# Kernel optimization log

Measured on AMD Instinct MI355X. Metric: run time of the kernel, lower is better.

## Reference

```python
import jax, jax.numpy as jnp
import numpy as np

B, S, D, H = 4, 4096, 512, 8


def setup_inputs() -> dict:
    key = jax.random.key(0)
    ks = jax.random.split(key, 9)
    s = 1.0 / np.sqrt(D)
    return {
        "x": jax.random.normal(ks[0], (B, S, D), jnp.float32),
        "Wq": jax.random.normal(ks[1], (D, D), jnp.float32) * s,
        "bq": jax.random.normal(ks[2], (D,), jnp.float32) * 0.02,
        "Wk": jax.random.normal(ks[3], (D, D), jnp.float32) * s,
        "bk": jax.random.normal(ks[4], (D,), jnp.float32) * 0.02,
        "Wv": jax.random.normal(ks[5], (D, D), jnp.float32) * s,
        "bv": jax.random.normal(ks[6], (D,), jnp.float32) * 0.02,
        "Wo": jax.random.normal(ks[7], (H * D, D), jnp.float32) * (1.0 / np.sqrt(H * D)),
        "bo": jax.random.normal(ks[8], (D,), jnp.float32) * 0.02,
        "num_heads": H,
    }


def reference(x, Wq, bq, Wk, bk, Wv, bv, Wo, bo, num_heads):
    # Q/K/V projections (self-attention path; encoder_output=None)
    q = x @ Wq + bq  # [B,S,D]
    k = x @ Wk + bk
    v = x @ Wv + bv
    scale = 1.0 / jnp.sqrt(jnp.asarray(x.shape[-1], x.dtype))
    scores = jnp.einsum("bqd,bkd->bqk", q, k) * scale  # [B,S,S]
    probs = jax.nn.softmax(scores, axis=-1)
    attn = jnp.einsum("bqk,bkd->bqd", probs, v)  # [B,S,D]
    # Original stacks identical heads then torch.cat along dim=-1 -> tile H copies.
    cat = jnp.tile(attn, (1, 1, num_heads))  # [B,S,H*D]
    return cat @ Wo + bo  # [B,S,D]
```

## Files before the change

kernel.cpp:

```cpp
#include <hip/hip_runtime.h>
#include <stdint.h>

#define SCALE 0.04419417382415922f

typedef __bf16 bf16x8 __attribute__((ext_vector_type(8)));
typedef float f32x4 __attribute__((ext_vector_type(4)));
typedef uint16_t u16x8 __attribute__((ext_vector_type(8)));

static __device__ __forceinline__ uint16_t f2bf(float f) {
  union { float f; uint32_t u; } v; v.f = f;
  uint32_t u = v.u;
  return (uint16_t)((u + 0x7FFFu + ((u >> 16) & 1u)) >> 16);
}
static __device__ __forceinline__ float bf2f(uint16_t h) {
  union { uint32_t u; float f; } v; v.u = ((uint32_t)h) << 16;
  return v.f;
}

static __device__ __forceinline__ void gload16(const void* g, void* l) {
  __builtin_amdgcn_global_load_lds(
      (__attribute__((address_space(1))) void*)g,
      (__attribute__((address_space(3))) void*)l, 16, 0, 0);
}

#define P_BAR asm volatile("s_barrier" ::: "memory")
#define P_LGKM do { asm volatile("s_waitcnt lgkmcnt(0)" ::: "memory"); \
                    __builtin_amdgcn_sched_barrier(0); } while (0)


__global__ __launch_bounds__(256)
void convert_x(const float* __restrict__ x, uint16_t* __restrict__ xb) {
  size_t i = ((size_t)blockIdx.x * 256 + threadIdx.x) * 8;
  float4 a = *(const float4*)(x + i);
  float4 b = *(const float4*)(x + i + 4);
  u16x8 o;
  o[0] = f2bf(a.x); o[1] = f2bf(a.y); o[2] = f2bf(a.z); o[3] = f2bf(a.w);
  o[4] = f2bf(b.x); o[5] = f2bf(b.y); o[6] = f2bf(b.z); o[7] = f2bf(b.w);
  *(u16x8*)(xb + i) = o;
}

__global__ __launch_bounds__(256)
void pack_wraw(const float* __restrict__ Wq, const float* __restrict__ Wk,
               const float* __restrict__ Wv,
               uint16_t* __restrict__ oq, uint16_t* __restrict__ ok,
               uint16_t* __restrict__ ov) {
  size_t i = ((size_t)blockIdx.x * 256 + threadIdx.x) * 8;
  const int m = blockIdx.y;
  const float* src = (m == 0) ? Wq : ((m == 1) ? Wk : Wv);
  uint16_t* dst = (m == 0) ? oq : ((m == 1) ? ok : ov);
  const float scl = (m == 0) ? SCALE : 1.0f;
  float4 a = *(const float4*)(src + i);
  float4 b = *(const float4*)(src + i + 4);
  u16x8 o;
  o[0] = f2bf(a.x * scl); o[1] = f2bf(a.y * scl);
  o[2] = f2bf(a.z * scl); o[3] = f2bf(a.w * scl);
  o[4] = f2bf(b.x * scl); o[5] = f2bf(b.y * scl);
  o[6] = f2bf(b.z * scl); o[7] = f2bf(b.w * scl);
  *(u16x8*)(dst + i) = o;
}

__global__ __launch_bounds__(256)
void pack_wo(const float* __restrict__ Wo, uint16_t* __restrict__ woT) {
  __shared__ float tile[64][65];
  const int k0 = blockIdx.x * 64, n0 = blockIdx.y * 64;
  const int t = threadIdx.x, r = t >> 2, c0 = (t & 3) * 16;
  float av[16];
  #pragma unroll
  for (int e = 0; e < 16; e++) av[e] = 0.f;
  for (int h = 0; h < 8; h++) {
    const float* src = &Wo[(size_t)(h * 512 + k0 + r) * 512 + n0 + c0];
    #pragma unroll
    for (int j = 0; j < 4; j++) {
      float4 v = *(const float4*)(src + j * 4);
      av[j * 4 + 0] += v.x; av[j * 4 + 1] += v.y;
      av[j * 4 + 2] += v.z; av[j * 4 + 3] += v.w;
    }
  }
  #pragma unroll
  for (int e = 0; e < 16; e++) tile[r][c0 + e] = av[e];
  __syncthreads();
  u16x8 o0, o1;
  #pragma unroll
  for (int e = 0; e < 8; e++) {
    o0[e] = f2bf(tile[c0 + e][r]);
    o1[e] = f2bf(tile[c0 + 8 + e][r]);
  }
  uint16_t* dst = woT + (size_t)(n0 + r) * 512 + k0 + c0;
  *(u16x8*)dst = o0;
  *(u16x8*)(dst + 8) = o1;
}

__global__ __launch_bounds__(256)
void gemv_g(const float* __restrict__ Wk, const float* __restrict__ bq,
            float* __restrict__ g) {
  __shared__ float vs[512];
  const int t = threadIdx.x;
  vs[t] = bq[t]; vs[t + 256] = bq[t + 256];
  __syncthreads();
  const int r = blockIdx.x * 32 + (t >> 3), j = t & 7;
  const float4* p = (const float4*)(Wk + (size_t)r * 512 + j * 64);
  float s = 0.f;
  #pragma unroll
  for (int q = 0; q < 16; q++) {
    float4 v = p[q];
    const float* b = &vs[j * 64 + q * 4];
    s += v.x * b[0] + v.y * b[1] + v.z * b[2] + v.w * b[3];
  }
  s += __shfl_xor(s, 1); s += __shfl_xor(s, 2); s += __shfl_xor(s, 4);
  if (j == 0) g[r] = s * SCALE;
}

__global__ __launch_bounds__(256)
void kappa_calc(const float* __restrict__ bq, const float* __restrict__ bk,
                float* __restrict__ g) {
  const int t = threadIdx.x;
  float s = bq[t] * bk[t] + bq[t + 256] * bk[t + 256];
  #pragma unroll
  for (int o = 32; o; o >>= 1) s += __shfl_xor(s, o);
  __shared__ float rr[4];
  if ((t & 63) == 0) rr[t >> 6] = s;
  __syncthreads();
  if (t == 0) g[512] = (rr[0] + rr[1] + rr[2] + rr[3]) * SCALE;
}

__global__ __launch_bounds__(256)
void gemv_bvo(const uint16_t* __restrict__ woT, const float* __restrict__ bv,
              float* __restrict__ out) {
  __shared__ float vs[512];
  const int t = threadIdx.x;
  vs[t] = bv[t]; vs[t + 256] = bv[t + 256];
  __syncthreads();
  const int r = blockIdx.x * 32 + (t >> 3), j = t & 7;
  const u16x8* p = (const u16x8*)(woT + (size_t)r * 512 + j * 64);
  float s = 0.f;
  #pragma unroll
  for (int q = 0; q < 8; q++) {
    u16x8 v = p[q];
    #pragma unroll
    for (int e = 0; e < 8; e++) s += bf2f(v[e]) * vs[j * 64 + q * 8 + e];
  }
  s += __shfl_xor(s, 1); s += __shfl_xor(s, 2); s += __shfl_xor(s, 4);
  if (j == 0) out[r] = s;
}

__global__ __launch_bounds__(256)
void c_vec(const uint16_t* __restrict__ xb, const float* __restrict__ g,
           float* __restrict__ cv) {
  __shared__ float gs[513];
  const int t = threadIdx.x;
  for (int i = t; i < 513; i += 256) gs[i] = g[i];
  __syncthreads();
  const int r = blockIdx.x * 32 + (t >> 3);
  const int j = t & 7;
  const uint16_t* p = xb + (size_t)r * 512 + j * 64;
  float s = 0.f;
  #pragma unroll
  for (int q = 0; q < 8; q++) {
    u16x8 v = *(const u16x8*)(p + q * 8);
    #pragma unroll
    for (int e = 0; e < 8; e++) s += bf2f(v[e]) * gs[j * 64 + q * 8 + e];
  }
  s += __shfl_xor(s, 1); s += __shfl_xor(s, 2); s += __shfl_xor(s, 4);
  if (j == 0) cv[r] = s + gs[512];
}

__global__ __launch_bounds__(256)
void transpose_v(const uint16_t* __restrict__ yv, uint16_t* __restrict__ Vt) {
  __shared__ uint16_t tile[64][72];
  const int s0 = blockIdx.x * 64, d0 = blockIdx.y * 64, b = blockIdx.z;
  const int t = threadIdx.x, r = t >> 2, c0 = (t & 3) * 16;
  const uint16_t* src = yv + ((size_t)(b * 4096 + s0 + r)) * 1024 + 512 + d0 + c0;
  *(u16x8*)&tile[r][c0] = *(const u16x8*)src;
  *(u16x8*)&tile[r][c0 + 8] = *(const u16x8*)(src + 8);
  __syncthreads();
  u16x8 o0, o1;
  #pragma unroll
  for (int e = 0; e < 8; e++) { o0[e] = tile[c0 + e][r]; o1[e] = tile[c0 + 8 + e][r]; }
  uint16_t* dst = Vt + ((size_t)b * 512 + d0 + r) * 4096 + s0 + c0;
  *(u16x8*)dst = o0;
  *(u16x8*)(dst + 8) = o1;
}

template<int BN, int MODE>
static __device__ __forceinline__
void gemm8_body(const uint16_t* __restrict__ A, const uint16_t* __restrict__ Bt,
                const float* __restrict__ bias, void* __restrict__ Cout,
                const float* __restrict__ sums,
                int M, int N, int K, int lda, int ldb, int ldc,
                long long aZ, long long bZ, long long cZ, long long sZ,
                long long biasZ) {
  constexpr int NREP = BN / 64;
  constexpr int NH = NREP / 2;
  constexpr int WN = BN / 4;
  constexpr int BELTS = BN * 64;
  __shared__ uint16_t SH[32768 + 2 * BELTS];

  const int nbn = N / BN;
  const int nwg = (M >> 8) * nbn;
  int id = blockIdx.x;
  id = (id & 7) * (nwg >> 3) + (id >> 3);
  const int bm = id / nbn, bn = id % nbn;
  const long long z = blockIdx.z;
  A += z * aZ; Bt += z * bZ;
  const size_t m0 = (size_t)bm * 256, n0 = (size_t)bn * BN;

  const int t = threadIdx.x;
  const int lane = t & 63, w = t >> 6;
  const int wr = w >> 2, wc = w & 3;
  const int l15 = lane & 15, l4 = lane >> 4, l7 = lane & 7, l3 = lane >> 3;
  const int sw = l7 ^ l3;

  const uint16_t* srcA = A + (m0 + w * 8 + l3) * (size_t)lda + sw * 8;
  const uint16_t* srcB = (BN == 256)
      ? Bt + (n0 + (w >> 1) * 64 + (w & 1) * 16 + l3) * (size_t)ldb + sw * 8
      : Bt + (n0 + (w >> 1) * 32 + (w & 1) * 8 + l3) * (size_t)ldb + sw * 8;

  const int NKT = K >> 6;
  const int NIT = NKT >> 1;

  f32x4 acc[8][NREP];
  #pragma unroll
  for (int i = 0; i < 8; i++)
    #pragma unroll
    for (int j = 0; j < NREP; j++) acc[i][j] = (f32x4)(0.f);

  bf16x8 a[4][2], b0[NH][2], b1[NH][2];

  auto stageA = [&](int tile, int mh) {
    const uint16_t* s = srcA + mh * 64 * (size_t)lda + tile * 64;
    uint16_t* d = SH + (tile & 1) * 16384 + mh * 4096 + w * 512;
    gload16(s, d);
    gload16(s + 128 * (size_t)lda, d + 8192);
  };
  auto stageB = [&](int tile, int nh) {
    if (BN == 256) {
      const uint16_t* s = srcB + nh * 32 * (size_t)ldb + tile * 64;
      uint16_t* d = SH + 32768 + (tile & 1) * BELTS + (w >> 1) * 4096 + nh * 2048 + (w & 1) * 1024;
      gload16(s, d);
      gload16(s + 8 * (size_t)ldb, d + 512);
    } else {
      const uint16_t* s = srcB + nh * 16 * (size_t)ldb + tile * 64;
      uint16_t* d = SH + 32768 + (tile & 1) * BELTS + (w >> 1) * 2048 + nh * 1024 + (w & 1) * 512;
      gload16(s, d);
    }
  };
  auto loadA = [&](int buf, int mh) {
    const uint16_t* base = SH + buf * 16384 + (wr * 128 + mh * 64 + l15) * 64;
    #pragma unroll
    for (int m = 0; m < 4; m++)
      #pragma unroll
      for (int ks = 0; ks < 2; ks++)
        a[m][ks] = *(const bf16x8*)(base + m * 1024 + (((ks * 4 + l4) ^ l7) * 8));
  };
  auto loadB = [&](int buf, int nh, bf16x8 (&bd)[NH][2]) {
    const uint16_t* base = SH + 32768 + buf * BELTS + (wc * WN + nh * (WN / 2) + l15) * 64;
    #pragma unroll
    for (int n = 0; n < NH; n++)
      #pragma unroll
      for (int ks = 0; ks < 2; ks++)
        bd[n][ks] = *(const bf16x8*)(base + n * 1024 + (((ks * 4 + l4) ^ l7) * 8));
  };
  auto quad = [&](int mh, int nq, bf16x8 (&bq)[NH][2]) {
    __builtin_amdgcn_s_setprio(1);
    #pragma unroll
    for (int m = 0; m < 4; m++)
      #pragma unroll
      for (int n = 0; n < NH; n++)
        #pragma unroll
        for (int ks = 0; ks < 2; ks++)
          acc[mh * 4 + m][nq + n] = __builtin_amdgcn_mfma_f32_16x16x32_bf16(
              a[m][ks], bq[n][ks], acc[mh * 4 + m][nq + n], 0, 0, 0);
    __builtin_amdgcn_s_setprio(0);
  };

  stageA(0, 0); stageB(0, 0); stageA(0, 1); stageB(0, 1);
  stageA(1, 0); stageB(1, 0); stageA(1, 1);
  if (BN == 256) asm volatile("s_waitcnt vmcnt(6)" ::: "memory");
  else           asm volatile("s_waitcnt vmcnt(5)" ::: "memory");
  P_BAR;

  for (int k = 0; k < NIT - 1; ++k) {
    const int tt = 2 * k;
    loadA(0, 0); loadB(0, 0, b0); stageB(tt + 1, 1);
    P_BAR; P_LGKM; quad(0, 0, b0); P_BAR;
    loadB(0, 1, b1); stageA(tt + 2, 0);
    P_BAR; P_LGKM; quad(0, NH, b1); P_BAR;
    loadA(0, 1); stageB(tt + 2, 0);
    P_BAR; P_LGKM; quad(1, NH, b1); P_BAR;
    stageA(tt + 2, 1);
    if (BN == 256) asm volatile("s_waitcnt vmcnt(6)" ::: "memory");
    else           asm volatile("s_waitcnt vmcnt(5)" ::: "memory");
    P_BAR; quad(1, 0, b0); P_BAR;
    loadA(1, 0); loadB(1, 0, b0); stageB(tt + 2, 1);
    P_BAR; P_LGKM; quad(0, 0, b0); P_BAR;
    loadB(1, 1, b1); stageA(tt + 3, 0);
    P_BAR; P_LGKM; quad(0, NH, b1); P_BAR;
    loadA(1, 1); stageB(tt + 3, 0);
    P_BAR; P_LGKM; quad(1, NH, b1); P_BAR;
    stageA(tt + 3, 1);
    if (BN == 256) asm volatile("s_waitcnt vmcnt(6)" ::: "memory");
    else           asm volatile("s_waitcnt vmcnt(5)" ::: "memory");
    P_BAR; quad(1, 0, b0); P_BAR;
  }
  loadA(0, 0); loadB(0, 0, b0); stageB(NKT - 1, 1);
  P_BAR; P_LGKM; quad(0, 0, b0); P_BAR;
  loadB(0, 1, b1);
  P_BAR; P_LGKM; quad(0, NH, b1); P_BAR;
  loadA(0, 1);
  P_BAR; P_LGKM; quad(1, NH, b1); P_BAR;
  asm volatile("s_waitcnt vmcnt(0)" ::: "memory");
  P_BAR; quad(1, 0, b0); P_BAR;
  loadA(1, 0); loadB(1, 0, b0);
  P_BAR; P_LGKM; quad(0, 0, b0); P_BAR;
  loadB(1, 1, b1);
  P_BAR; P_LGKM; quad(0, NH, b1); P_BAR;
  loadA(1, 1);
  P_BAR; P_LGKM; quad(1, NH, b1); P_BAR;
  quad(1, 0, b0);

  asm volatile("s_waitcnt vmcnt(0) lgkmcnt(0)" ::: "memory");
  __syncthreads();

  const int g = l4;

  if (MODE == 1 || MODE == 4) {
    float bvv[NREP];
    #pragma unroll
    for (int ni = 0; ni < NREP; ni++) bvv[ni] = bias[n0 + wc * WN + ni * 16 + l15];
    float4 sc[8];
    if (MODE == 4) {
      #pragma unroll
      for (int am = 0; am < 8; am++)
        sc[am] = *(const float4*)&sums[z * sZ + m0 + wr * 128 + am * 16 + g * 4];
    }
    float* C = (float*)Cout + z * cZ;
    #pragma unroll
    for (int am = 0; am < 8; am++)
      #pragma unroll
      for (int r = 0; r < 4; r++) {
        size_t gr = m0 + wr * 128 + am * 16 + g * 4 + r;
        #pragma unroll
        for (int ni = 0; ni < NREP; ni++) {
          float v = acc[am][ni][r];
          if (MODE == 4) v *= ((const float*)&sc[am])[r];
          C[gr * (size_t)ldc + n0 + wc * WN + ni * 16 + l15] = v + bvv[ni];
        }
      }
    return;
  }

  if (MODE == 2) {
    float cvv[NREP];
    #pragma unroll
    for (int ni = 0; ni < NREP; ni++)
      cvv[ni] = bias[z * biasZ + n0 + wc * WN + ni * 16 + l15];
    #pragma unroll
    for (int am = 0; am < 8; am++)
      #pragma unroll
      for (int r = 0; r < 4; r++) {
        float s = 0.f;
        #pragma unroll
        for (int ni = 0; ni < NREP; ni++) {
          float v = __expf(acc[am][ni][r] + cvv[ni]);
          acc[am][ni][r] = v;
          s += v;
        }
        s += __shfl_xor(s, 1); s += __shfl_xor(s, 2);
        s += __shfl_xor(s, 4); s += __shfl_xor(s, 8);
        if (l15 == 0)
          ((float*)sums)[z * sZ + (m0 + wr * 128 + am * 16 + g * 4 + r) * 64 +
                         (n0 >> 6) + wc] = s;
      }
  }

  float bvv[NREP];
  #pragma unroll
  for (int ni = 0; ni < NREP; ni++)
    bvv[ni] = (MODE == 0 && bias) ? bias[n0 + wc * WN + ni * 16 + l15] : 0.f;

  constexpr int STR = BN + 8;
  uint16_t* C16 = (uint16_t*)Cout + z * cZ;
  #pragma unroll
  for (int h = 0; h < 2; ++h) {
    __syncthreads();
    if (wr == h) {
      #pragma unroll
      for (int am = 0; am < 8; am++)
        #pragma unroll
        for (int r = 0; r < 4; r++) {
          const int lr = am * 16 + g * 4 + r;
          #pragma unroll
          for (int ni = 0; ni < NREP; ni++) {
            float v = acc[am][ni][r] + bvv[ni];
            SH[lr * STR + wc * WN + ni * 16 + l15] = f2bf(v);
          }
        }
    }
    __syncthreads();
    constexpr int CPT = BN / 32;
    #pragma unroll
    for (int c = 0; c < CPT; ++c) {
      const int idx = t + c * 512;
      const int row = idx / (BN / 8), c8 = idx % (BN / 8);
      *(u16x8*)(C16 + (m0 + h * 128 + row) * (size_t)ldc + n0 + c8 * 8) =
          *(const u16x8*)(SH + row * STR + c8 * 8);
    }
  }
}

__global__ __launch_bounds__(512, 2)
void w2_gemm(const uint16_t* A, const uint16_t* Bt, void* C) {
  gemm8_body<128, 0>(A, Bt, nullptr, C, nullptr, 512, 512, 512, 512, 512, 512,
                     0, 0, 0, 0, 0);
}
__global__ __launch_bounds__(512, 2)
void wvo_gemm(const uint16_t* A, const uint16_t* Bt, void* C) {
  gemm8_body<128, 0>(A, Bt, nullptr, C, nullptr, 512, 512, 512, 512, 512, 512,
                     0, 0, 0, 0, 0);
}
__global__ __launch_bounds__(512, 2)
void yv_gemm(const uint16_t* A, const uint16_t* Bt, const float* bias, void* C) {
  gemm8_body<256, 0>(A, Bt, bias, C, nullptr, 16384, 1024, 512, 512, 512, 1024,
                     0, 0, 0, 0, 0);
}
__global__ __launch_bounds__(512, 2)
void scores_gemm(const uint16_t* Y, const uint16_t* X, const float* cvec,
                 void* S, float* sums) {
  gemm8_body<256, 2>(Y, X, cvec, S, sums, 4096, 4096, 512, 1024, 512, 4096,
                     (long long)4096 * 1024, (long long)4096 * 512,
                     (long long)4096 * 4096, (long long)4096 * 64, 4096);
}
__global__ __launch_bounds__(512, 2)
void pvo_gemm(const uint16_t* A, const uint16_t* Bt, const float* bias,
              void* C, const float* inv) {
  gemm8_body<128, 4>(A, Bt, bias, C, inv, 4096, 512, 4096, 4096, 4096, 512,
                     (long long)4096 * 4096, (long long)512 * 4096,
                     (long long)4096 * 512, 4096, 0);
}

__global__ __launch_bounds__(256)
void reduce_sums(const float* __restrict__ P, float* __restrict__ inv, int rows) {
  int r = blockIdx.x * 256 + threadIdx.x;
  if (r >= rows) return;
  const float4* p4 = (const float4*)(P + (size_t)r * 64);
  float s = 0.f;
  #pragma unroll
  for (int i = 0; i < 16; ++i) { float4 v = p4[i]; s += (v.x + v.y) + (v.z + v.w); }
  inv[r] = 1.f / s;
}


extern "C" void kernel_launch(void* const* d_in, const int* in_sizes, int n_in,
                              void* d_out, int out_size, void* d_ws, size_t ws_size,
                              hipStream_t stream) {
  const float* x   = (const float*)d_in[0];
  const float* Wq  = (const float*)d_in[1];
  const float* bq  = (const float*)d_in[2];
  const float* Wk  = (const float*)d_in[3];
  const float* bk  = (const float*)d_in[4];
  const float* Wv  = (const float*)d_in[5];
  const float* bvp = (const float*)d_in[6];
  const float* Wo  = (const float*)d_in[7];
  const float* bo  = (const float*)d_in[8];
  float* out = (float*)d_out;

  char* ws = (char*)d_ws;
  const size_t MB = (size_t)1 << 20;
  uint16_t* xb   = (uint16_t*)(ws);
  uint16_t* yv   = (uint16_t*)(ws + 16 * MB);
  uint16_t* Vt   = (uint16_t*)(ws + 48 * MB);
  uint16_t* wqs  = (uint16_t*)(ws + 80 * MB);
  uint16_t* wkr  = (uint16_t*)(ws + 80 * MB + 512 * 1024);
  uint16_t* yvW  = (uint16_t*)(ws + 81 * MB);
  uint16_t* w2T  = yvW;
  uint16_t* wvoT = yvW + (size_t)512 * 512;
  uint16_t* woT  = (uint16_t*)(ws + 82 * MB);
  uint16_t* wvr  = (uint16_t*)(ws + 82 * MB + 512 * 1024);
  float*    byv  = (float*)   (ws + 83 * MB);
  float*    g    = (float*)   (ws + 83 * MB + 8 * 1024);
  float*    sums = (float*)   (ws + 84 * MB);
  float*    invs = (float*)   (ws + 88 * MB);
  float*    cv   = (float*)   (ws + 89 * MB);
  uint16_t* Sbuf = (uint16_t*)(ws + 96 * MB);

  const int big = (ws_size >= 225 * MB);

  convert_x<<<dim3(4096), dim3(256), 0, stream>>>(x, xb);
  pack_wraw<<<dim3(128, 3), dim3(256), 0, stream>>>(Wq, Wk, Wv, wqs, wkr, wvr);
  pack_wo<<<dim3(8, 8), dim3(256), 0, stream>>>(Wo, woT);
  gemv_g<<<dim3(16), dim3(256), 0, stream>>>(Wk, bq, g);
  kappa_calc<<<dim3(1), dim3(256), 0, stream>>>(bq, bk, g);
  hipMemsetAsync(byv, 0, 512 * sizeof(float), stream);
  gemv_bvo<<<dim3(16), dim3(256), 0, stream>>>(woT, bvp, byv + 512);

  w2_gemm<<<dim3(8, 1, 1), dim3(512), 0, stream>>>(wkr, wqs, w2T);
  wvo_gemm<<<dim3(8, 1, 1), dim3(512), 0, stream>>>(woT, wvr, wvoT);

  yv_gemm<<<dim3(256, 1, 1), dim3(512), 0, stream>>>(xb, yvW, byv, yv);

  transpose_v<<<dim3(64, 8, 4), dim3(256), 0, stream>>>(yv, Vt);
  c_vec<<<dim3(512), dim3(256), 0, stream>>>(xb, g, cv);

  if (big) {
    for (int p = 0; p < 2; ++p) {
      scores_gemm<<<dim3(256, 1, 2), dim3(512), 0, stream>>>(
          yv + (size_t)p * 2 * 4096 * 1024, xb + (size_t)p * 2 * 4096 * 512,
          cv + (size_t)p * 2 * 4096, Sbuf + (size_t)p * 2 * 4096 * 4096,
          sums + (size_t)p * 2 * 4096 * 64);
      reduce_sums<<<dim3(2 * 4096 / 256), dim3(256), 0, stream>>>(
          sums + (size_t)p * 2 * 4096 * 64, invs + (size_t)p * 2 * 4096, 2 * 4096);
    }
    pvo_gemm<<<dim3(64, 1, 4), dim3(512), 0, stream>>>(Sbuf, Vt, bo, out, invs);
  } else {
    for (int p = 0; p < 2; ++p) {
      scores_gemm<<<dim3(256, 1, 2), dim3(512), 0, stream>>>(
          yv + (size_t)p * 2 * 4096 * 1024, xb + (size_t)p * 2 * 4096 * 512,
          cv + (size_t)p * 2 * 4096, Sbuf,
          sums + (size_t)p * 2 * 4096 * 64);
      reduce_sums<<<dim3(2 * 4096 / 256), dim3(256), 0, stream>>>(
          sums + (size_t)p * 2 * 4096 * 64, invs + (size_t)p * 2 * 4096, 2 * 4096);
      pvo_gemm<<<dim3(64, 1, 2), dim3(512), 0, stream>>>(
          Sbuf, Vt + (size_t)p * 2 * 512 * 4096, bo,
          out + (size_t)p * 2 * 4096 * 512, invs + (size_t)p * 2 * 4096);
    }
  }
}
```

Measured before the change: 282.5 us.

## Fuse scores, softmax and PV into a single flash-attention style kernel

```diff
diff --git a/kernel.cpp b/kernel.cpp
--- a/kernel.cpp
+++ b/kernel.cpp
@@ -185,10 +185,7 @@
 static __device__ __forceinline__
 void gemm8_body(const uint16_t* __restrict__ A, const uint16_t* __restrict__ Bt,
                 const float* __restrict__ bias, void* __restrict__ Cout,
-                const float* __restrict__ sums,
-                int M, int N, int K, int lda, int ldb, int ldc,
-                long long aZ, long long bZ, long long cZ, long long sZ,
-                long long biasZ) {
+                int M, int N, int K, int lda, int ldb, int ldc) {
   constexpr int NREP = BN / 64;
   constexpr int NH = NREP / 2;
   constexpr int WN = BN / 4;
@@ -200,8 +197,6 @@
   int id = blockIdx.x;
   id = (id & 7) * (nwg >> 3) + (id >> 3);
   const int bm = id / nbn, bn = id % nbn;
-  const long long z = blockIdx.z;
-  A += z * aZ; Bt += z * bZ;
   const size_t m0 = (size_t)bm * 256, n0 = (size_t)bn * BN;
 
   const int t = threadIdx.x;
@@ -322,64 +317,13 @@
   __syncthreads();
 
   const int g = l4;
-
-  if (MODE == 1 || MODE == 4) {
-    float bvv[NREP];
-    #pragma unroll
-    for (int ni = 0; ni < NREP; ni++) bvv[ni] = bias[n0 + wc * WN + ni * 16 + l15];
-    float4 sc[8];
-    if (MODE == 4) {
-      #pragma unroll
-      for (int am = 0; am < 8; am++)
-        sc[am] = *(const float4*)&sums[z * sZ + m0 + wr * 128 + am * 16 + g * 4];
-    }
-    float* C = (float*)Cout + z * cZ;
-    #pragma unroll
-    for (int am = 0; am < 8; am++)
-      #pragma unroll
-      for (int r = 0; r < 4; r++) {
-        size_t gr = m0 + wr * 128 + am * 16 + g * 4 + r;
-        #pragma unroll
-        for (int ni = 0; ni < NREP; ni++) {
-          float v = acc[am][ni][r];
-          if (MODE == 4) v *= ((const float*)&sc[am])[r];
-          C[gr * (size_t)ldc + n0 + wc * WN + ni * 16 + l15] = v + bvv[ni];
-        }
-      }
-    return;
-  }
-
-  if (MODE == 2) {
-    float cvv[NREP];
-    #pragma unroll
-    for (int ni = 0; ni < NREP; ni++)
-      cvv[ni] = bias[z * biasZ + n0 + wc * WN + ni * 16 + l15];
-    #pragma unroll
-    for (int am = 0; am < 8; am++)
-      #pragma unroll
-      for (int r = 0; r < 4; r++) {
-        float s = 0.f;
-        #pragma unroll
-        for (int ni = 0; ni < NREP; ni++) {
-          float v = __expf(acc[am][ni][r] + cvv[ni]);
-          acc[am][ni][r] = v;
-          s += v;
-        }
-        s += __shfl_xor(s, 1); s += __shfl_xor(s, 2);
-        s += __shfl_xor(s, 4); s += __shfl_xor(s, 8);
-        if (l15 == 0)
-          ((float*)sums)[z * sZ + (m0 + wr * 128 + am * 16 + g * 4 + r) * 64 +
-                         (n0 >> 6) + wc] = s;
-      }
-  }
-
   float bvv[NREP];
   #pragma unroll
   for (int ni = 0; ni < NREP; ni++)
-    bvv[ni] = (MODE == 0 && bias) ? bias[n0 + wc * WN + ni * 16 + l15] : 0.f;
+    bvv[ni] = (bias != nullptr) ? bias[n0 + wc * WN + ni * 16 + l15] : 0.f;
 
   constexpr int STR = BN + 8;
-  uint16_t* C16 = (uint16_t*)Cout + z * cZ;
+  uint16_t* C16 = (uint16_t*)Cout;
   #pragma unroll
   for (int h = 0; h < 2; ++h) {
     __syncthreads();
@@ -390,10 +334,8 @@
         for (int r = 0; r < 4; r++) {
           const int lr = am * 16 + g * 4 + r;
           #pragma unroll
-          for (int ni = 0; ni < NREP; ni++) {
-            float v = acc[am][ni][r] + bvv[ni];
-            SH[lr * STR + wc * WN + ni * 16 + l15] = f2bf(v);
-          }
+          for (int ni = 0; ni < NREP; ni++)
+            SH[lr * STR + wc * WN + ni * 16 + l15] = f2bf(acc[am][ni][r] + bvv[ni]);
         }
     }
     __syncthreads();
@@ -410,43 +352,192 @@
 
 __global__ __launch_bounds__(512, 2)
 void w2_gemm(const uint16_t* A, const uint16_t* Bt, void* C) {
-  gemm8_body<128, 0>(A, Bt, nullptr, C, nullptr, 512, 512, 512, 512, 512, 512,
-                     0, 0, 0, 0, 0);
+  gemm8_body<128, 0>(A, Bt, nullptr, C, 512, 512, 512, 512, 512, 512);
 }
 __global__ __launch_bounds__(512, 2)
 void wvo_gemm(const uint16_t* A, const uint16_t* Bt, void* C) {
-  gemm8_body<128, 0>(A, Bt, nullptr, C, nullptr, 512, 512, 512, 512, 512, 512,
-                     0, 0, 0, 0, 0);
+  gemm8_body<128, 0>(A, Bt, nullptr, C, 512, 512, 512, 512, 512, 512);
 }
 __global__ __launch_bounds__(512, 2)
 void yv_gemm(const uint16_t* A, const uint16_t* Bt, const float* bias, void* C) {
-  gemm8_body<256, 0>(A, Bt, bias, C, nullptr, 16384, 1024, 512, 512, 512, 1024,
-                     0, 0, 0, 0, 0);
-}
+  gemm8_body<256, 0>(A, Bt, bias, C, 16384, 1024, 512, 512, 512, 1024);
+}
+
 __global__ __launch_bounds__(512, 2)
-void scores_gemm(const uint16_t* Y, const uint16_t* X, const float* cvec,
-                 void* S, float* sums) {
-  gemm8_body<256, 2>(Y, X, cvec, S, sums, 4096, 4096, 512, 1024, 512, 4096,
-                     (long long)4096 * 1024, (long long)4096 * 512,
-                     (long long)4096 * 4096, (long long)4096 * 64, 4096);
-}
-__global__ __launch_bounds__(512, 2)
-void pvo_gemm(const uint16_t* A, const uint16_t* Bt, const float* bias,
-              void* C, const float* inv) {
-  gemm8_body<128, 4>(A, Bt, bias, C, inv, 4096, 512, 4096, 4096, 4096, 512,
-                     (long long)4096 * 4096, (long long)512 * 4096,
-                     (long long)4096 * 512, 4096, 0);
-}
-
-__global__ __launch_bounds__(256)
-void reduce_sums(const float* __restrict__ P, float* __restrict__ inv, int rows) {
-  int r = blockIdx.x * 256 + threadIdx.x;
-  if (r >= rows) return;
-  const float4* p4 = (const float4*)(P + (size_t)r * 64);
-  float s = 0.f;
-  #pragma unroll
-  for (int i = 0; i < 16; ++i) { float4 v = p4[i]; s += (v.x + v.y) + (v.z + v.w); }
-  inv[r] = 1.f / s;
+void fa_fused(const uint16_t* __restrict__ yv, const uint16_t* __restrict__ xb,
+              const uint16_t* __restrict__ Vt, const float* __restrict__ cv,
+              const float* __restrict__ bo, float* __restrict__ out) {
+  __shared__ __align__(16) uint16_t SH[53248];
+  uint16_t* XL = SH;
+  uint16_t* PL = SH + 16384;
+  uint16_t* VL = SH + 20480;
+
+  const int bid = blockIdx.x;
+  const int id = ((bid & 7) << 3) | (bid >> 3);
+  const long long z = blockIdx.z;
+  const size_t m0 = (size_t)id * 64;
+  const int t = threadIdx.x, lane = t & 63, w = t >> 6;
+  const int wr = w >> 2, wc = w & 3;
+  const int l15 = lane & 15, l4 = lane >> 4, l7 = lane & 7, l3 = lane >> 3;
+  const int sw = l7 ^ l3;
+
+  const uint16_t* Yz = yv + z * (4096ll * 1024);
+  const uint16_t* Xz = xb + z * (4096ll * 512);
+  const uint16_t* Vz = Vt + z * (512ll * 4096);
+  const float*    cz = cv + z * 4096;
+  float*          oz = out + z * (4096ll * 512);
+
+  bf16x8 a_y[2][16];
+  #pragma unroll
+  for (int mi = 0; mi < 2; mi++) {
+    const uint16_t* yp = Yz + (m0 + wr * 32 + mi * 16 + l15) * 1024 + l4 * 8;
+    #pragma unroll
+    for (int kg = 0; kg < 16; kg++)
+      a_y[mi][kg] = *(const bf16x8*)(yp + kg * 32);
+  }
+
+  f32x4 acc[2][8];
+  #pragma unroll
+  for (int i = 0; i < 2; i++)
+    #pragma unroll
+    for (int j = 0; j < 8; j++) acc[i][j] = (f32x4)(0.f);
+  float ps[2][4];
+  #pragma unroll
+  for (int i = 0; i < 2; i++)
+    #pragma unroll
+    for (int r = 0; r < 4; r++) ps[i][r] = 0.f;
+
+  const uint16_t* xsrc = Xz + (w * 8 + l3) * 512 + sw * 8;
+  const uint16_t* vsrc = Vz + (size_t)(w * 8 + l3) * 4096 + sw * 8;
+  uint16_t* xdst = XL + w * 512;
+  uint16_t* vdst = VL + w * 512;
+
+  auto stage_x = [&](int T, int dk, int buf) {
+    const uint16_t* s = xsrc + (size_t)T * 64 * 512 + dk * 128;
+    gload16(s,      xdst + buf * 8192);
+    gload16(s + 64, xdst + buf * 8192 + 4096);
+  };
+  auto stage_v = [&](int s0, int c) {
+    gload16(vsrc + (size_t)c * 64 * 4096 + s0, vdst + c * 4096);
+  };
+
+  stage_x(0, 0, 0);
+  asm volatile("s_waitcnt vmcnt(0)" ::: "memory");
+  P_BAR;
+
+  #pragma unroll 1
+  for (int T = 0; T < 64; ++T) {
+    const int s0 = T * 64;
+    f32x4 acc_s[2];
+    acc_s[0] = (f32x4)(0.f); acc_s[1] = (f32x4)(0.f);
+
+    #pragma unroll
+    for (int dk = 0; dk < 4; ++dk) {
+      const int buf = dk & 1;
+      stage_v(s0, dk * 2);
+      stage_v(s0, dk * 2 + 1);
+      if (dk < 3) stage_x(T, dk + 1, buf ^ 1);
+      else        stage_x(T + 1, 0, buf ^ 1);
+      asm volatile("s_waitcnt vmcnt(4)" ::: "memory");
+      P_BAR;
+      bf16x8 bx[4];
+      #pragma unroll
+      for (int ks = 0; ks < 4; ks++)
+        bx[ks] = *(const bf16x8*)(XL + buf * 8192 + (ks >> 1) * 4096 +
+                                  (wc * 16 + l15) * 64 +
+                                  ((((ks & 1) * 4 + l4) ^ l7) * 8));
+      P_LGKM;
+      __builtin_amdgcn_s_setprio(1);
+      #pragma unroll
+      for (int mi = 0; mi < 2; mi++)
+        #pragma unroll
+        for (int ks = 0; ks < 4; ks++)
+          acc_s[mi] = __builtin_amdgcn_mfma_f32_16x16x32_bf16(
+              a_y[mi][dk * 4 + ks], bx[ks], acc_s[mi], 0, 0, 0);
+      __builtin_amdgcn_s_setprio(0);
+      P_BAR;
+    }
+
+    const float cq = cz[s0 + wc * 16 + l15];
+    #pragma unroll
+    for (int mi = 0; mi < 2; mi++) {
+      const int qb = wr * 32 + mi * 16 + l4 * 4;
+      #pragma unroll
+      for (int r = 0; r < 4; r++) {
+        float p = __expf(acc_s[mi][r] + cq);
+        ps[mi][r] += p;
+        const int qr = qb + r;
+        PL[qr * 64 + (((wc * 2 + (l15 >> 3)) ^ (qr & 7)) * 8) + l7] = f2bf(p);
+      }
+    }
+    P_LGKM;
+    asm volatile("s_waitcnt vmcnt(2)" ::: "memory");
+    P_BAR;
+
+    bf16x8 pa[2][2];
+    #pragma unroll
+    for (int m = 0; m < 2; m++)
+      #pragma unroll
+      for (int ks = 0; ks < 2; ks++)
+        pa[m][ks] = *(const bf16x8*)(PL + (wr * 32 + m * 16 + l15) * 64 +
+                                     (((ks * 4 + l4) ^ l7) * 8));
+    #pragma unroll
+    for (int h = 0; h < 2; h++) {
+      bf16x8 vb[4][2];
+      #pragma unroll
+      for (int n = 0; n < 4; n++)
+        #pragma unroll
+        for (int ks = 0; ks < 2; ks++)
+          vb[n][ks] = *(const bf16x8*)(VL + (wc * 128 + (h * 4 + n) * 16 + l15) * 64 +
+                                       (((ks * 4 + l4) ^ l7) * 8));
+      P_LGKM;
+      __builtin_amdgcn_s_setprio(1);
+      #pragma unroll
+      for (int m = 0; m < 2; m++)
+        #pragma unroll
+        for (int n = 0; n < 4; n++)
+          #pragma unroll
+          for (int ks = 0; ks < 2; ks++)
+            acc[m][h * 4 + n] = __builtin_amdgcn_mfma_f32_16x16x32_bf16(
+                pa[m][ks], vb[n][ks], acc[m][h * 4 + n], 0, 0, 0);
+      __builtin_amdgcn_s_setprio(0);
+    }
+    P_BAR;
+  }
+
+  asm volatile("s_waitcnt vmcnt(0) lgkmcnt(0)" ::: "memory");
+  __syncthreads();
+  float* rs = (float*)SH;
+  #pragma unroll
+  for (int mi = 0; mi < 2; mi++)
+    #pragma unroll
+    for (int r = 0; r < 4; r++) {
+      float s = ps[mi][r];
+      s += __shfl_xor(s, 1); s += __shfl_xor(s, 2);
+      s += __shfl_xor(s, 4); s += __shfl_xor(s, 8);
+      if (l15 == 0) rs[wc * 64 + wr * 32 + mi * 16 + l4 * 4 + r] = s;
+    }
+  __syncthreads();
+  float inv[2][4];
+  #pragma unroll
+  for (int mi = 0; mi < 2; mi++)
+    #pragma unroll
+    for (int r = 0; r < 4; r++) {
+      const int q = wr * 32 + mi * 16 + l4 * 4 + r;
+      inv[mi][r] = 1.f / (((rs[q] + rs[64 + q]) + (rs[128 + q] + rs[192 + q])));
+    }
+  float bvv[8];
+  #pragma unroll
+  for (int n = 0; n < 8; n++) bvv[n] = bo[wc * 128 + n * 16 + l15];
+  #pragma unroll
+  for (int mi = 0; mi < 2; mi++)
+    #pragma unroll
+    for (int r = 0; r < 4; r++) {
+      float* op = oz + (m0 + wr * 32 + mi * 16 + l4 * 4 + r) * 512 + wc * 128 + l15;
+      #pragma unroll
+      for (int n = 0; n < 8; n++)
+        op[n * 16] = acc[mi][n][r] * inv[mi][r] + bvv[n];
+    }
 }
 
 
@@ -478,12 +569,7 @@
   uint16_t* wvr  = (uint16_t*)(ws + 82 * MB + 512 * 1024);
   float*    byv  = (float*)   (ws + 83 * MB);
   float*    g    = (float*)   (ws + 83 * MB + 8 * 1024);
-  float*    sums = (float*)   (ws + 84 * MB);
-  float*    invs = (float*)   (ws + 88 * MB);
-  float*    cv   = (float*)   (ws + 89 * MB);
-  uint16_t* Sbuf = (uint16_t*)(ws + 96 * MB);
-
-  const int big = (ws_size >= 225 * MB);
+  float*    cv   = (float*)   (ws + 84 * MB);
 
   convert_x<<<dim3(4096), dim3(256), 0, stream>>>(x, xb);
   pack_wraw<<<dim3(128, 3), dim3(256), 0, stream>>>(Wq, Wk, Wv, wqs, wkr, wvr);
@@ -501,27 +587,5 @@
   transpose_v<<<dim3(64, 8, 4), dim3(256), 0, stream>>>(yv, Vt);
   c_vec<<<dim3(512), dim3(256), 0, stream>>>(xb, g, cv);
 
-  if (big) {
-    for (int p = 0; p < 2; ++p) {
-      scores_gemm<<<dim3(256, 1, 2), dim3(512), 0, stream>>>(
-          yv + (size_t)p * 2 * 4096 * 1024, xb + (size_t)p * 2 * 4096 * 512,
-          cv + (size_t)p * 2 * 4096, Sbuf + (size_t)p * 2 * 4096 * 4096,
-          sums + (size_t)p * 2 * 4096 * 64);
-      reduce_sums<<<dim3(2 * 4096 / 256), dim3(256), 0, stream>>>(
-          sums + (size_t)p * 2 * 4096 * 64, invs + (size_t)p * 2 * 4096, 2 * 4096);
-    }
-    pvo_gemm<<<dim3(64, 1, 4), dim3(512), 0, stream>>>(Sbuf, Vt, bo, out, invs);
-  } else {
-    for (int p = 0; p < 2; ++p) {
-      scores_gemm<<<dim3(256, 1, 2), dim3(512), 0, stream>>>(
-          yv + (size_t)p * 2 * 4096 * 1024, xb + (size_t)p * 2 * 4096 * 512,
-          cv + (size_t)p * 2 * 4096, Sbuf,
-          sums + (size_t)p * 2 * 4096 * 64);
-      reduce_sums<<<dim3(2 * 4096 / 256), dim3(256), 0, stream>>>(
-          sums + (size_t)p * 2 * 4096 * 64, invs + (size_t)p * 2 * 4096, 2 * 4096);
-      pvo_gemm<<<dim3(64, 1, 2), dim3(512), 0, stream>>>(
-          Sbuf, Vt + (size_t)p * 2 * 512 * 4096, bo,
-          out + (size_t)p * 2 * 4096 * 512, invs + (size_t)p * 2 * 4096);
-    }
-  }
-}
+  fa_fused<<<dim3(64, 1, 4), dim3(512), 0, stream>>>(yv, xb, Vt, cv, bo, out);
+}
```

New measurement: 366.1 us. 1.3x slower.
